# Performance work log

Measured on AMD Instinct MI355X. Metric: run time of the kernel, lower is better.

## Reference

```python
import jax, jax.numpy as jnp
import numpy as np

B, S, K, N = 4, 2048, 4096, 4096


def setup_inputs() -> dict:
    key = jax.random.key(0)
    kx, kw = jax.random.split(key)
    # int8 activations and weights in [-127, 127), matching torch.randint(-127,127,...)
    x = jax.random.randint(kx, (B, S, K), -127, 127, dtype=jnp.int32).astype(jnp.int8)
    weight = jax.random.randint(kw, (N, K), -127, 127, dtype=jnp.int32).astype(jnp.int8)
    bias = jnp.zeros((1, N), dtype=jnp.int32)
    out_scale = jnp.ones((), dtype=jnp.float32)
    bias_scale = jnp.ones((), dtype=jnp.float32)
    return {"x": x, "weight": weight, "bias": bias,
            "out_scale": out_scale, "bias_scale": bias_scale}


def reference(x, weight, bias, out_scale, bias_scale):
    # Flatten leading dims: [B, S, K] -> [M, K]
    x_shape = x.shape
    x2 = x.reshape(-1, x_shape[-1])
    acc = jax.lax.dot_general(
        x2, weight,
        dimension_numbers=(((1,), (1,)), ((), ())),
        preferred_element_type=jnp.int32,
    )  # [M, N] int32
    # Fused epilogue: y = round(out_scale * acc + bias_scale * bias) -> int32
    y = jnp.round(acc.astype(jnp.float32) * out_scale
                  + bias.astype(jnp.float32) * bias_scale).astype(jnp.int32)
    return y.reshape(*x_shape[:-1], -1)
```

## Files before the change

kernel.cpp:

```cpp
#include <hip/hip_runtime.h>
#include <stdint.h>


typedef int v4i __attribute__((ext_vector_type(4)));

#define BM 128
#define BN 128
#define BK 128
#define KK 4096

__global__ __launch_bounds__(256)
void pack_i32_to_i8(const v4i* __restrict__ src, int* __restrict__ dst, int n4) {
    int i = blockIdx.x * blockDim.x + threadIdx.x;
    if (i >= n4) return;
    v4i a = src[i];
    dst[i] = (a[0] & 0xff) | ((a[1] & 0xff) << 8) | ((a[2] & 0xff) << 16) | (a[3] << 24);
}

__device__ __forceinline__ void gld_lds16(const void* g, void* lds) {
    __builtin_amdgcn_global_load_lds(
        (const __attribute__((address_space(1))) unsigned int*)g,
        (__attribute__((address_space(3))) unsigned int*)lds,
        16, 0, 0);
}

__global__ __launch_bounds__(256, 2)
void w8a8_gemm_kernel(const int8_t* __restrict__ X,
                      const int8_t* __restrict__ W,
                      const int*    __restrict__ bias,
                      const float*  __restrict__ out_scale_p,
                      const float*  __restrict__ bias_scale_p,
                      int*          __restrict__ Y,
                      int M, int N)
{
    __shared__ __align__(16) int8_t sA[BM * BK];
    __shared__ __align__(16) int8_t sB[BN * BK];

    const int t = threadIdx.x;
    const int w = t >> 6;
    const int l = t & 63;
    const int wm = w >> 1;
    const int wn = w & 1;

    const int bn = blockIdx.x * BN;
    const int bm = blockIdx.y * BM;

    const float out_scale  = *out_scale_p;
    const float bias_scale = *bias_scale_p;

    const int8_t* Abase = X + (size_t)bm * KK;
    const int8_t* Bbase = W + (size_t)bn * KK;

    int ga[4];
#pragma unroll
    for (int r = 0; r < 4; r++) {
        const int c   = r * 256 + w * 64 + l;
        const int row = c >> 3;
        const int j   = c & 7;
        ga[r] = row * KK + ((j ^ (row & 7)) << 4);
    }

    const int tm   = l & 15;
    const int quad = l >> 4;
    const int s3   = tm & 7;
    const int rowA = (wm * 64 + tm) * BK;
    const int rowB = (wn * 64 + tm) * BK;

    v4i acc[4][4];
    const v4i vzero = {0, 0, 0, 0};
#pragma unroll
    for (int i = 0; i < 4; i++)
#pragma unroll
        for (int j = 0; j < 4; j++)
            acc[i][j] = vzero;

    for (int k0 = 0; k0 < KK; k0 += BK) {
#pragma unroll
        for (int r = 0; r < 4; r++) {
            gld_lds16(Abase + ga[r] + k0, sA + r * 4096 + w * 1024);
            gld_lds16(Bbase + ga[r] + k0, sB + r * 4096 + w * 1024);
        }
        __syncthreads();

#pragma unroll
        for (int h = 0; h < 2; h++) {
            const int xo = (((h << 2) + quad) ^ s3) << 4;
            v4i a[4], b[4];
#pragma unroll
            for (int i = 0; i < 4; i++)
                a[i] = *(const v4i*)(sA + rowA + i * 16 * BK + xo);
#pragma unroll
            for (int j = 0; j < 4; j++)
                b[j] = *(const v4i*)(sB + rowB + j * 16 * BK + xo);
#pragma unroll
            for (int i = 0; i < 4; i++)
#pragma unroll
                for (int j = 0; j < 4; j++)
                    acc[i][j] = __builtin_amdgcn_mfma_i32_16x16x64_i8(a[i], b[j], acc[i][j], 0, 0, 0);
        }

        __syncthreads();
    }

#pragma unroll
    for (int j = 0; j < 4; j++) {
        const int n = bn + wn * 64 + j * 16 + tm;
        const float bb = (float)bias[n] * bias_scale;
#pragma unroll
        for (int i = 0; i < 4; i++) {
            const int mb = bm + wm * 64 + i * 16 + quad * 4;
#pragma unroll
            for (int r = 0; r < 4; r++) {
                const float v = (float)acc[i][j][r] * out_scale + bb;
                Y[(size_t)(mb + r) * N + n] = (int)rintf(v);
            }
        }
    }
}

extern "C" void kernel_launch(void* const* d_in, const int* in_sizes, int n_in,
                              void* d_out, int out_size, void* d_ws, size_t ws_size,
                              hipStream_t stream) {
    const int* x32 = (const int*)d_in[0];
    const int* w32 = (const int*)d_in[1];
    const int*    bias = (const int*)d_in[2];
    const float*  os   = (const float*)d_in[3];
    const float*  bs   = (const float*)d_in[4];
    int* out = (int*)d_out;

    const int K = KK;
    const int M = in_sizes[0] / K;
    const int N = in_sizes[1] / K;
    const int nx = in_sizes[0];
    const int nw = in_sizes[1];

    int8_t* x8 = (int8_t*)d_ws;
    int8_t* w8 = x8 + (size_t)nx;

    pack_i32_to_i8<<<dim3(nx / 4 / 256), dim3(256), 0, stream>>>((const v4i*)x32, (int*)x8, nx / 4);
    pack_i32_to_i8<<<dim3(nw / 4 / 256), dim3(256), 0, stream>>>((const v4i*)w32, (int*)w8, nw / 4);

    dim3 grid(N / BN, M / BM);
    dim3 block(256);
    hipLaunchKernelGGL(w8a8_gemm_kernel, grid, block, 0, stream,
                       x8, w8, bias, os, bs, out, M, N);
}
```

Baseline: 392.5 us.

## Use 256x256 tiles with double-buffered LDS pipeline and swizzled block order

Tiles grow to 256x256 with 512 threads (8 waves, 2x4), and each wave now computes a 128x64 sub-tile. LDS is double-buffered and global-to-LDS loads for the next K-step are interleaved with MFMA phases, using explicit vmcnt waits, barriers and s_setprio. A 1D grid with a remapped block order is added for the 16x32 tile grid to improve L2 locality. The aim is to hide load latency behind MFMA work and raise arithmetic intensity, at the cost of more registers (128 accumulator VGPRs plus fragments) and 128KB of LDS per block, which may cut occupancy.

Result: slower. 415.2 us (+5.8%).

```diff
diff --git a/kernel.cpp b/kernel.cpp
--- a/kernel.cpp
+++ b/kernel.cpp
@@ -4,10 +4,11 @@
 
 typedef int v4i __attribute__((ext_vector_type(4)));
 
-#define BM 128
-#define BN 128
+#define BM 256
+#define BN 256
 #define BK 128
 #define KK 4096
+#define KT (KK / BK)
 
 __global__ __launch_bounds__(256)
 void pack_i32_to_i8(const v4i* __restrict__ src, int* __restrict__ dst, int n4) {
@@ -24,7 +25,12 @@
         16, 0, 0);
 }
 
-__global__ __launch_bounds__(256, 2)
+#define MFMA_I8 __builtin_amdgcn_mfma_i32_16x16x64_i8
+#define BARRIER() __builtin_amdgcn_s_barrier()
+#define LGKM0() asm volatile("s_waitcnt lgkmcnt(0)" ::: "memory")
+#define PRIO(x) __builtin_amdgcn_s_setprio(x)
+
+__global__ __launch_bounds__(512, 2)
 void w8a8_gemm_kernel(const int8_t* __restrict__ X,
                       const int8_t* __restrict__ W,
                       const int*    __restrict__ bias,
@@ -33,17 +39,25 @@
                       int*          __restrict__ Y,
                       int M, int N)
 {
-    __shared__ __align__(16) int8_t sA[BM * BK];
-    __shared__ __align__(16) int8_t sB[BN * BK];
-
-    const int t = threadIdx.x;
-    const int w = t >> 6;
-    const int l = t & 63;
-    const int wm = w >> 1;
-    const int wn = w & 1;
-
-    const int bn = blockIdx.x * BN;
-    const int bm = blockIdx.y * BM;
+    __shared__ __align__(16) int8_t sA[2 * BM * BK];
+    __shared__ __align__(16) int8_t sB[2 * BN * BK];
+
+    const int tid = threadIdx.x;
+
+    const int nbx = N / BN;
+    const int nby = M / BM;
+    int bx, by;
+    {
+        const int wg = blockIdx.x;
+        if (nbx == 16 && nby == 32) {
+            const int x = wg & 7;
+            const int k = wg >> 3;
+            bx = ((x & 1) << 3) | (k & 7);
+            by = ((x >> 1) << 3) | (k >> 3);
+        } else { bx = wg % nbx; by = wg / nbx; }
+    }
+    const int bn = bx * BN;
+    const int bm = by * BM;
 
     const float out_scale  = *out_scale_p;
     const float bias_scale = *bias_scale_p;
@@ -51,66 +65,144 @@
     const int8_t* Abase = X + (size_t)bm * KK;
     const int8_t* Bbase = W + (size_t)bn * KK;
 
-    int ga[4];
-#pragma unroll
-    for (int r = 0; r < 4; r++) {
-        const int c   = r * 256 + w * 64 + l;
-        const int row = c >> 3;
-        const int j   = c & 7;
-        ga[r] = row * KK + ((j ^ (row & 7)) << 4);
-    }
-
+    const int r0  = tid >> 3;
+    const int j0  = tid & 7;
+    const int sw  = (j0 ^ (r0 & 7)) << 4;
+    const size_t gOff = (size_t)r0 * KK + sw;
+    const int  lOff = tid << 4;
+
+#define STAGE(gbase, lds, t, h) do {                                              \
+        const int8_t* _g = (gbase) + (size_t)((h) * 128) * KK                     \
+                                   + (size_t)(t) * BK + gOff;                     \
+        int8_t* _l = (lds) + (((t) & 1) << 15) + ((h) << 14) + lOff;              \
+        gld_lds16(_g,                  _l);                                       \
+        gld_lds16(_g + (size_t)64 * KK, _l + 8192);                               \
+    } while (0)
+
+    const int w    = tid >> 6;
+    const int l    = tid & 63;
+    const int wmw  = w >> 2;
+    const int wnw  = w & 3;
     const int tm   = l & 15;
     const int quad = l >> 4;
     const int s3   = tm & 7;
-    const int rowA = (wm * 64 + tm) * BK;
-    const int rowB = (wn * 64 + tm) * BK;
-
-    v4i acc[4][4];
-    const v4i vzero = {0, 0, 0, 0};
-#pragma unroll
-    for (int i = 0; i < 4; i++)
-#pragma unroll
-        for (int j = 0; j < 4; j++)
-            acc[i][j] = vzero;
-
-    for (int k0 = 0; k0 < KK; k0 += BK) {
-#pragma unroll
-        for (int r = 0; r < 4; r++) {
-            gld_lds16(Abase + ga[r] + k0, sA + r * 4096 + w * 1024);
-            gld_lds16(Bbase + ga[r] + k0, sB + r * 4096 + w * 1024);
-        }
-        __syncthreads();
-
-#pragma unroll
-        for (int h = 0; h < 2; h++) {
-            const int xo = (((h << 2) + quad) ^ s3) << 4;
-            v4i a[4], b[4];
-#pragma unroll
-            for (int i = 0; i < 4; i++)
-                a[i] = *(const v4i*)(sA + rowA + i * 16 * BK + xo);
-#pragma unroll
-            for (int j = 0; j < 4; j++)
-                b[j] = *(const v4i*)(sB + rowB + j * 16 * BK + xo);
-#pragma unroll
-            for (int i = 0; i < 4; i++)
-#pragma unroll
-                for (int j = 0; j < 4; j++)
-                    acc[i][j] = __builtin_amdgcn_mfma_i32_16x16x64_i8(a[i], b[j], acc[i][j], 0, 0, 0);
-        }
-
-        __syncthreads();
+    const int xo0  = ( quad      ^ s3) << 4;
+    const int xo1  = ((quad + 4) ^ s3) << 4;
+    const int rowA = ((wmw << 7) + tm) << 7;
+    const int rowB = ((wnw << 6) + tm) << 7;
+
+    v4i acc[8][4];
+    const v4i vz = {0, 0, 0, 0};
+#pragma unroll
+    for (int i = 0; i < 8; ++i)
+#pragma unroll
+        for (int j = 0; j < 4; ++j)
+            acc[i][j] = vz;
+
+    STAGE(Abase, sA, 0, 0); STAGE(Abase, sA, 0, 1);
+    STAGE(Bbase, sB, 0, 0); STAGE(Bbase, sB, 0, 1);
+    STAGE(Abase, sA, 1, 0); STAGE(Abase, sA, 1, 1);
+    asm volatile("s_waitcnt vmcnt(4)" ::: "memory");
+    BARRIER();
+
+#pragma unroll 2
+    for (int t = 0; t < KT; ++t) {
+        const int bo = (t & 1) << 15;
+        const int8_t* sAb = sA + bo;
+        const int8_t* sBb = sB + bo;
+        v4i aF[8][2], bL[2][2], bH[2][2];
+
+#pragma unroll
+        for (int i = 0; i < 4; ++i) {
+            aF[i][0] = *(const v4i*)(sAb + rowA + i * 2048 + xo0);
+            aF[i][1] = *(const v4i*)(sAb + rowA + i * 2048 + xo1);
+        }
+#pragma unroll
+        for (int j = 0; j < 2; ++j) {
+            bL[j][0] = *(const v4i*)(sBb + rowB + j * 2048 + xo0);
+            bL[j][1] = *(const v4i*)(sBb + rowB + j * 2048 + xo1);
+        }
+        if (t + 1 < KT) STAGE(Bbase, sB, t + 1, 0);
+        BARRIER();
+        LGKM0();
+        PRIO(1);
+#pragma unroll
+        for (int i = 0; i < 4; ++i)
+#pragma unroll
+            for (int j = 0; j < 2; ++j) {
+                acc[i][j] = MFMA_I8(aF[i][0], bL[j][0], acc[i][j], 0, 0, 0);
+                acc[i][j] = MFMA_I8(aF[i][1], bL[j][1], acc[i][j], 0, 0, 0);
+            }
+        PRIO(0);
+        BARRIER();
+
+#pragma unroll
+        for (int i = 4; i < 8; ++i) {
+            aF[i][0] = *(const v4i*)(sAb + rowA + i * 2048 + xo0);
+            aF[i][1] = *(const v4i*)(sAb + rowA + i * 2048 + xo1);
+        }
+        if (t + 1 < KT) STAGE(Bbase, sB, t + 1, 1);
+        BARRIER();
+        LGKM0();
+        PRIO(1);
+#pragma unroll
+        for (int i = 4; i < 8; ++i)
+#pragma unroll
+            for (int j = 0; j < 2; ++j) {
+                acc[i][j] = MFMA_I8(aF[i][0], bL[j][0], acc[i][j], 0, 0, 0);
+                acc[i][j] = MFMA_I8(aF[i][1], bL[j][1], acc[i][j], 0, 0, 0);
+            }
+        PRIO(0);
+        BARRIER();
+
+#pragma unroll
+        for (int j = 0; j < 2; ++j) {
+            bH[j][0] = *(const v4i*)(sBb + rowB + (j + 2) * 2048 + xo0);
+            bH[j][1] = *(const v4i*)(sBb + rowB + (j + 2) * 2048 + xo1);
+        }
+        if (t + 2 < KT) STAGE(Abase, sA, t + 2, 0);
+        BARRIER();
+        LGKM0();
+        PRIO(1);
+#pragma unroll
+        for (int i = 0; i < 4; ++i)
+#pragma unroll
+            for (int j = 0; j < 2; ++j) {
+                acc[i][j + 2] = MFMA_I8(aF[i][0], bH[j][0], acc[i][j + 2], 0, 0, 0);
+                acc[i][j + 2] = MFMA_I8(aF[i][1], bH[j][1], acc[i][j + 2], 0, 0, 0);
+            }
+        PRIO(0);
+        BARRIER();
+
+        if (t + 2 < KT) {
+            STAGE(Abase, sA, t + 2, 1);
+            asm volatile("s_waitcnt vmcnt(4)" ::: "memory");
+        } else {
+            asm volatile("s_waitcnt vmcnt(0)" ::: "memory");
+        }
+        BARRIER();
+        PRIO(1);
+#pragma unroll
+        for (int i = 4; i < 8; ++i)
+#pragma unroll
+            for (int j = 0; j < 2; ++j) {
+                acc[i][j + 2] = MFMA_I8(aF[i][0], bH[j][0], acc[i][j + 2], 0, 0, 0);
+                acc[i][j + 2] = MFMA_I8(aF[i][1], bH[j][1], acc[i][j + 2], 0, 0, 0);
+            }
+        PRIO(0);
+        BARRIER();
     }
-
-#pragma unroll
-    for (int j = 0; j < 4; j++) {
-        const int n = bn + wn * 64 + j * 16 + tm;
+#undef STAGE
+
+#pragma unroll
+    for (int j = 0; j < 4; ++j) {
+        const int n = bn + (wnw << 6) + (j << 4) + tm;
         const float bb = (float)bias[n] * bias_scale;
 #pragma unroll
-        for (int i = 0; i < 4; i++) {
-            const int mb = bm + wm * 64 + i * 16 + quad * 4;
-#pragma unroll
-            for (int r = 0; r < 4; r++) {
+        for (int i = 0; i < 8; ++i) {
+            const int mb = bm + (wmw << 7) + (i << 4) + (quad << 2);
+#pragma unroll
+            for (int r = 0; r < 4; ++r) {
                 const float v = (float)acc[i][j][r] * out_scale + bb;
                 Y[(size_t)(mb + r) * N + n] = (int)rintf(v);
             }
@@ -140,8 +232,8 @@
     pack_i32_to_i8<<<dim3(nx / 4 / 256), dim3(256), 0, stream>>>((const v4i*)x32, (int*)x8, nx / 4);
     pack_i32_to_i8<<<dim3(nw / 4 / 256), dim3(256), 0, stream>>>((const v4i*)w32, (int*)w8, nw / 4);
 
-    dim3 grid(N / BN, M / BM);
-    dim3 block(256);
+    dim3 grid((N / BN) * (M / BM));
+    dim3 block(512);
     hipLaunchKernelGGL(w8a8_gemm_kernel, grid, block, 0, stream,
                        x8, w8, bias, os, bs, out, M, N);
 }
```
